# Kernel tuning notes

Measured on AMD Instinct MI355X. Metric: run time of the kernel, lower is better.

## Reference

```python
import jax, jax.numpy as jnp
import numpy as np

OUT, GROUPS, GRID = 4096, 1, 8   # 2^bits = 8 -> 3-bit codes
IN = 4096
B, S = 4, 2048

def setup_inputs() -> dict:
    key = jax.random.key(0)
    k1, k2, k3 = jax.random.split(key, 3)
    x = jax.random.normal(k1, (B, S, IN), dtype=jnp.float32)
    quant_grid = jax.random.normal(k2, (OUT, GROUPS, GRID), dtype=jnp.float32) * 0.02
    weight_codes = jax.random.randint(k3, (OUT, GROUPS, IN // GROUPS), 0, GRID, dtype=jnp.int32)
    return {"x": x, "quant_grid": quant_grid, "weight_codes": weight_codes}

def reference(x, quant_grid, weight_codes):
    # Dequantize: per-(row, group) codebook lookup -> full weight [OUT, IN]
    W = jnp.take_along_axis(quant_grid, weight_codes, axis=-1)  # [OUT, GROUPS, IN//GROUPS]
    W = W.reshape(W.shape[0], -1)                               # [OUT, IN]
    # y = X @ W.T
    return jnp.einsum('bsi,oi->bso', x, W)
```

## Files before the change

kernel.cpp:

```cpp
#include <hip/hip_runtime.h>


#define M_DIM 8192
#define N_DIM 4096
#define K_DIM 4096
#define BK 64
#define NKT (K_DIM / BK)

typedef __attribute__((ext_vector_type(4))) int int32x4;

#define AS1 __attribute__((address_space(1)))
#define AS3 __attribute__((address_space(3)))

__device__ __forceinline__ void gl_lds16(const void* g, void* l) {
    __builtin_amdgcn_global_load_lds((const AS1 void*)g, (AS3 void*)l, 16, 0, 0);
}

__global__ __launch_bounds__(256) void quant_x(const float* __restrict__ X,
                                               char* __restrict__ XQ,
                                               float* __restrict__ SX) {
    const int row = blockIdx.x;
    const int t = threadIdx.x;
    const float4* xp = (const float4*)(X + (size_t)row * K_DIM);
    float4 v[4];
    float mx = 0.0f;
#pragma unroll
    for (int i = 0; i < 4; ++i) {
        v[i] = xp[t * 4 + i];
        mx = fmaxf(mx, fmaxf(fmaxf(fabsf(v[i].x), fabsf(v[i].y)),
                             fmaxf(fabsf(v[i].z), fabsf(v[i].w))));
    }
#pragma unroll
    for (int off = 1; off < 64; off <<= 1)
        mx = fmaxf(mx, __shfl_xor(mx, off));
    __shared__ float wmx[4];
    if ((t & 63) == 0) wmx[t >> 6] = mx;
    __syncthreads();
    mx = fmaxf(fmaxf(wmx[0], wmx[1]), fmaxf(wmx[2], wmx[3]));
    const float inv = 127.0f / mx;
    int4 o4;
    int* po = (int*)&o4;
#pragma unroll
    for (int i = 0; i < 4; ++i) {
        int q0 = (int)rintf(v[i].x * inv);
        int q1 = (int)rintf(v[i].y * inv);
        int q2 = (int)rintf(v[i].z * inv);
        int q3 = (int)rintf(v[i].w * inv);
        po[i] = (q0 & 255) | ((q1 & 255) << 8) | ((q2 & 255) << 16) | ((q3 & 255) << 24);
    }
    const int mpanel = row >> 6, mf = (row >> 4) & 3, fr = row & 15;
    const int kp = t >> 2, kg = t & 3;
    ((int4*)XQ)[(size_t)mpanel * 16384 + kp * 256 + mf * 64 + kg * 16 + fr] = o4;
    if (t == 0) SX[row] = mx * (1.0f / 127.0f);
}

__global__ __launch_bounds__(256) void quant_w(const int* __restrict__ CD,
                                               const float* __restrict__ G,
                                               char* __restrict__ WQ,
                                               float* __restrict__ SW) {
    const int o = blockIdx.x;
    __shared__ int gq[8];
    if (threadIdx.x == 0) {
        float g[8], mx = 0.0f;
#pragma unroll
        for (int j = 0; j < 8; ++j) { g[j] = G[o * 8 + j]; mx = fmaxf(mx, fabsf(g[j])); }
        mx = fmaxf(mx, 1e-20f);
        const float inv = 127.0f / mx;
        SW[o] = mx * (1.0f / 127.0f);
#pragma unroll
        for (int j = 0; j < 8; ++j) gq[j] = ((int)rintf(g[j] * inv)) & 255;
    }
    __syncthreads();
    const int4* cp = (const int4*)(CD + (size_t)o * K_DIM);
    int* wp = (int*)(WQ + (size_t)o * K_DIM);
#pragma unroll
    for (int r = 0; r < 4; ++r) {
        int idx = r * 256 + threadIdx.x;
        int4 c = cp[idx];
        wp[idx] = gq[c.x] | (gq[c.y] << 8) | (gq[c.z] << 16) | (gq[c.w] << 24);
    }
}

__global__ __launch_bounds__(512, 4) void gemm8(const char* __restrict__ A,
                                                const char* __restrict__ B,
                                                const float* __restrict__ SX,
                                                const float* __restrict__ SW,
                                                float* __restrict__ C) {
    __shared__ char Bs[2][256 * 64];

    const int tid = threadIdx.x;
    const int lane = tid & 63;
    const int wid = tid >> 6;
    const int wm = wid >> 2;
    const int wn = wid & 3;

    int wg = blockIdx.x;
    wg = (wg & 7) * (gridDim.x >> 3) + (wg >> 3);
    const int ntn = N_DIM / 256;
    const int bm = (wg / ntn) * 128;
    const int bn = (wg % ntn) * 256;

    const int fr = lane & 15;
    const int g = lane >> 4;
    const int offk = fr * 64 + ((g ^ ((fr >> 1) & 3)) << 4);
    const int bwoff = wn * 4096;

    const char* Apan = A + (size_t)((bm >> 6) + wm) * 262144 + lane * 16;

    const int row0 = tid >> 2;
    const int sl = (((tid & 3) ^ ((row0 >> 1) & 3)) << 4);
    const char* gB0 = B + (size_t)(bn + row0) * K_DIM + sl;
    const char* gB1 = B + (size_t)(bn + 128 + row0) * K_DIM + sl;

#define KCL(KT) (((KT) < NKT) ? (KT) : 0)

#define STGB(BUF, KT) do {                                                         \
        const int kb_ = KCL(KT) * BK;                                              \
        gl_lds16(gB0 + kb_, &Bs[BUF][0] + wid * 1024);                             \
        gl_lds16(gB1 + kb_, &Bs[BUF][8192] + wid * 1024);                          \
    } while (0)

#define LDA(KT) do {                                                               \
        const char* ap_ = Apan + (size_t)KCL(KT) * 4096;                           \
        fa[0] = *(const int32x4*)(ap_);                                            \
        fa[1] = *(const int32x4*)(ap_ + 1024);                                     \
        fa[2] = *(const int32x4*)(ap_ + 2048);                                     \
        fa[3] = *(const int32x4*)(ap_ + 3072);                                     \
    } while (0)

#define RD_B(BUF)                                                                  \
    _Pragma("unroll") for (int n = 0; n < 4; ++n)                                  \
        fb[n] = *(const int32x4*)&Bs[BUF][bwoff + n * 1024 + offk];

#define MF_ALL                                                                     \
    _Pragma("unroll") for (int m = 0; m < 4; ++m)                                  \
    _Pragma("unroll") for (int n = 0; n < 4; ++n)                                  \
        acc[m][n] = __builtin_amdgcn_mfma_i32_16x16x64_i8(fa[m], fb[n], acc[m][n], 0, 0, 0);

#define BODY(CUR, KT) do {                                                         \
        RD_B(CUR)                                                                  \
        __builtin_amdgcn_s_setprio(1);                                             \
        MF_ALL                                                                     \
        __builtin_amdgcn_s_setprio(0);                                             \
        __builtin_amdgcn_sched_barrier(0);                                         \
        LDA((KT) + 1);                                                             \
        asm volatile("s_waitcnt vmcnt(4)" ::: "memory");                           \
        __builtin_amdgcn_s_barrier();                                              \
        STGB(CUR, (KT) + 2);                                                       \
    } while (0)

    int32x4 acc[4][4] = {};
    int32x4 fa[4];
    int32x4 fb[4];

    STGB(0, 0);
    STGB(1, 1);
    LDA(0);
    asm volatile("s_waitcnt vmcnt(4)" ::: "memory");
    __builtin_amdgcn_s_barrier();

    for (int j = 0; j < NKT / 2; ++j) {
        BODY(0, 2 * j);
        BODY(1, 2 * j + 1);
    }
    asm volatile("s_waitcnt vmcnt(0)" ::: "memory");

    const int crow0 = bm + wm * 64 + (g << 2);
    const int ccol0 = bn + wn * 64 + fr;
    float swc[4];
#pragma unroll
    for (int ni = 0; ni < 4; ++ni) swc[ni] = SW[ccol0 + ni * 16];
#pragma unroll
    for (int mi = 0; mi < 4; ++mi)
#pragma unroll
        for (int r = 0; r < 4; ++r) {
            const float sxr = SX[crow0 + mi * 16 + r];
#pragma unroll
            for (int ni = 0; ni < 4; ++ni)
                C[(size_t)(crow0 + mi * 16 + r) * N_DIM + ccol0 + ni * 16] =
                    (float)acc[mi][ni][r] * sxr * swc[ni];
        }
}

__global__ __launch_bounds__(256) void fb_gemm(const float* __restrict__ X,
                                               const float* __restrict__ G,
                                               const int* __restrict__ CD,
                                               float* __restrict__ Y) {
    __shared__ float xs[16][64];
    __shared__ float ws[16][64];
    const int bm = blockIdx.y << 6, bn = blockIdx.x << 6;
    const int tid = threadIdx.x;
    const int tn = tid & 15, tm = tid >> 4;
    float acc[4][4] = {};
    for (int k0 = 0; k0 < K_DIM; k0 += 16) {
#pragma unroll
        for (int r = 0; r < 4; ++r) {
            int e = r * 256 + tid;
            int mm = e >> 4, kk = e & 15;
            xs[kk][mm] = X[(size_t)(bm + mm) * K_DIM + k0 + kk];
            int code = CD[(size_t)(bn + mm) * K_DIM + k0 + kk];
            ws[kk][mm] = G[(bn + mm) * 8 + code];
        }
        __syncthreads();
#pragma unroll
        for (int kk = 0; kk < 16; ++kk)
#pragma unroll
            for (int i = 0; i < 4; ++i)
#pragma unroll
                for (int j = 0; j < 4; ++j)
                    acc[i][j] += xs[kk][tm * 4 + i] * ws[kk][tn * 4 + j];
        __syncthreads();
    }
#pragma unroll
    for (int i = 0; i < 4; ++i)
#pragma unroll
        for (int j = 0; j < 4; ++j)
            Y[(size_t)(bm + tm * 4 + i) * N_DIM + bn + tn * 4 + j] = acc[i][j];
}

extern "C" void kernel_launch(void* const* d_in, const int* in_sizes, int n_in,
                              void* d_out, int out_size, void* d_ws, size_t ws_size,
                              hipStream_t stream) {
    const float* x = (const float*)d_in[0];
    const float* qg = (const float*)d_in[1];
    const int* wc = (const int*)d_in[2];
    float* y = (float*)d_out;

    const size_t sx_off = 0;
    const size_t sw_off = (size_t)M_DIM * 4;
    const size_t xq_off = (size_t)(M_DIM + N_DIM) * 4;
    const size_t wq_off = xq_off + (size_t)M_DIM * K_DIM;
    const size_t need = wq_off + (size_t)N_DIM * K_DIM;

    if (ws_size >= need) {
        float* sx = (float*)((char*)d_ws + sx_off);
        float* sw = (float*)((char*)d_ws + sw_off);
        char* xq = (char*)d_ws + xq_off;
        char* wq = (char*)d_ws + wq_off;
        hipLaunchKernelGGL(quant_x, dim3(M_DIM), dim3(256), 0, stream, x, xq, sx);
        hipLaunchKernelGGL(quant_w, dim3(N_DIM), dim3(256), 0, stream, wc, qg, wq, sw);
        const int nwg = (M_DIM / 128) * (N_DIM / 256);
        hipLaunchKernelGGL(gemm8, dim3(nwg), dim3(512), 0, stream,
                           xq, wq, sx, sw, y);
    } else {
        hipLaunchKernelGGL(fb_gemm, dim3(N_DIM / 64, M_DIM / 64), dim3(256), 0, stream,
                           x, qg, wc, y);
    }
}
```

Before: 221.2 us.

## Stage A through LDS with 256x256 tiles and triple-buffered pipeline

```diff
diff --git a/kernel.cpp b/kernel.cpp
--- a/kernel.cpp
+++ b/kernel.cpp
@@ -48,9 +48,7 @@
         int q3 = (int)rintf(v[i].w * inv);
         po[i] = (q0 & 255) | ((q1 & 255) << 8) | ((q2 & 255) << 16) | ((q3 & 255) << 24);
     }
-    const int mpanel = row >> 6, mf = (row >> 4) & 3, fr = row & 15;
-    const int kp = t >> 2, kg = t & 3;
-    ((int4*)XQ)[(size_t)mpanel * 16384 + kp * 256 + mf * 64 + kg * 16 + fr] = o4;
+    ((int4*)(XQ + (size_t)row * K_DIM))[t] = o4;
     if (t == 0) SX[row] = mx * (1.0f / 127.0f);
 }
 
@@ -81,12 +79,14 @@
     }
 }
 
-__global__ __launch_bounds__(512, 4) void gemm8(const char* __restrict__ A,
+__global__ __launch_bounds__(512, 2) void gemm3(const char* __restrict__ A,
                                                 const char* __restrict__ B,
                                                 const float* __restrict__ SX,
                                                 const float* __restrict__ SW,
                                                 float* __restrict__ C) {
-    __shared__ char Bs[2][256 * 64];
+    __shared__ char As[3][256 * 64];
+    __shared__ char Bs[3][256 * 64];
+    __shared__ char Scr[16384];
 
     const int tid = threadIdx.x;
     const int lane = tid & 63;
@@ -97,81 +97,69 @@
     int wg = blockIdx.x;
     wg = (wg & 7) * (gridDim.x >> 3) + (wg >> 3);
     const int ntn = N_DIM / 256;
-    const int bm = (wg / ntn) * 128;
+    const int bm = (wg / ntn) * 256;
     const int bn = (wg % ntn) * 256;
 
     const int fr = lane & 15;
     const int g = lane >> 4;
     const int offk = fr * 64 + ((g ^ ((fr >> 1) & 3)) << 4);
-    const int bwoff = wn * 4096;
-
-    const char* Apan = A + (size_t)((bm >> 6) + wm) * 262144 + lane * 16;
 
     const int row0 = tid >> 2;
     const int sl = (((tid & 3) ^ ((row0 >> 1) & 3)) << 4);
+    const char* gA0 = A + (size_t)(bm + row0) * K_DIM + sl;
+    const char* gA1 = A + (size_t)(bm + 128 + row0) * K_DIM + sl;
     const char* gB0 = B + (size_t)(bn + row0) * K_DIM + sl;
     const char* gB1 = B + (size_t)(bn + 128 + row0) * K_DIM + sl;
 
-#define KCL(KT) (((KT) < NKT) ? (KT) : 0)
-
-#define STGB(BUF, KT) do {                                                         \
-        const int kb_ = KCL(KT) * BK;                                              \
-        gl_lds16(gB0 + kb_, &Bs[BUF][0] + wid * 1024);                             \
-        gl_lds16(gB1 + kb_, &Bs[BUF][8192] + wid * 1024);                          \
+#define STG_TO(DA, DB, KT) do {                                                    \
+        const int kb_ = (KT) * BK;                                                 \
+        gl_lds16(gA0 + kb_, (DA) + wid * 1024);                                    \
+        gl_lds16(gA1 + kb_, (DA) + 8192 + wid * 1024);                             \
+        gl_lds16(gB0 + kb_, (DB) + wid * 1024);                                    \
+        gl_lds16(gB1 + kb_, (DB) + 8192 + wid * 1024);                             \
     } while (0)
 
-#define LDA(KT) do {                                                               \
-        const char* ap_ = Apan + (size_t)KCL(KT) * 4096;                           \
-        fa[0] = *(const int32x4*)(ap_);                                            \
-        fa[1] = *(const int32x4*)(ap_ + 1024);                                     \
-        fa[2] = *(const int32x4*)(ap_ + 2048);                                     \
-        fa[3] = *(const int32x4*)(ap_ + 3072);                                     \
-    } while (0)
-
-#define RD_B(BUF)                                                                  \
-    _Pragma("unroll") for (int n = 0; n < 4; ++n)                                  \
-        fb[n] = *(const int32x4*)&Bs[BUF][bwoff + n * 1024 + offk];
-
-#define MF_ALL                                                                     \
-    _Pragma("unroll") for (int m = 0; m < 4; ++m)                                  \
-    _Pragma("unroll") for (int n = 0; n < 4; ++n)                                  \
-        acc[m][n] = __builtin_amdgcn_mfma_i32_16x16x64_i8(fa[m], fb[n], acc[m][n], 0, 0, 0);
-
-#define BODY(CUR, KT) do {                                                         \
-        RD_B(CUR)                                                                  \
-        __builtin_amdgcn_s_setprio(1);                                             \
-        MF_ALL                                                                     \
-        __builtin_amdgcn_s_setprio(0);                                             \
-        __builtin_amdgcn_sched_barrier(0);                                         \
-        LDA((KT) + 1);                                                             \
-        asm volatile("s_waitcnt vmcnt(4)" ::: "memory");                           \
-        __builtin_amdgcn_s_barrier();                                              \
-        STGB(CUR, (KT) + 2);                                                       \
-    } while (0)
-
-    int32x4 acc[4][4] = {};
-    int32x4 fa[4];
+    int32x4 acc[8][4] = {};
+    int32x4 fa[8];
     int32x4 fb[4];
 
-    STGB(0, 0);
-    STGB(1, 1);
-    LDA(0);
+    STG_TO(&As[0][0], &Bs[0][0], 0);
+    STG_TO(&As[1][0], &Bs[1][0], 1);
     asm volatile("s_waitcnt vmcnt(4)" ::: "memory");
     __builtin_amdgcn_s_barrier();
 
-    for (int j = 0; j < NKT / 2; ++j) {
-        BODY(0, 2 * j);
-        BODY(1, 2 * j + 1);
+    for (int t = 0; t < NKT; ++t) {
+        const int cur = t % 3;
+        {
+            const int s = t + 2;
+            char* da = (s < NKT) ? &As[s % 3][0] : &Scr[0];
+            char* db = (s < NKT) ? &Bs[s % 3][0] : &Scr[0];
+            STG_TO(da, db, (s < NKT) ? s : 0);
+        }
+#pragma unroll
+        for (int m = 0; m < 8; ++m)
+            fa[m] = *(const int32x4*)&As[cur][wm * 8192 + m * 1024 + offk];
+#pragma unroll
+        for (int n = 0; n < 4; ++n)
+            fb[n] = *(const int32x4*)&Bs[cur][wn * 4096 + n * 1024 + offk];
+#pragma unroll
+        for (int m = 0; m < 8; ++m)
+#pragma unroll
+            for (int n = 0; n < 4; ++n)
+                acc[m][n] = __builtin_amdgcn_mfma_i32_16x16x64_i8(
+                    fa[m], fb[n], acc[m][n], 0, 0, 0);
+        asm volatile("s_waitcnt vmcnt(4)" ::: "memory");
+        __builtin_amdgcn_s_barrier();
     }
     asm volatile("s_waitcnt vmcnt(0)" ::: "memory");
 
-    const int crow0 = bm + wm * 64 + (g << 2);
+    const int crow0 = bm + wm * 128 + (g << 2);
     const int ccol0 = bn + wn * 64 + fr;
     float swc[4];
 #pragma unroll
     for (int ni = 0; ni < 4; ++ni) swc[ni] = SW[ccol0 + ni * 16];
 #pragma unroll
-    for (int mi = 0; mi < 4; ++mi)
+    for (int mi = 0; mi < 8; ++mi)
 #pragma unroll
         for (int r = 0; r < 4; ++r) {
             const float sxr = SX[crow0 + mi * 16 + r];
@@ -239,8 +227,8 @@
         char* wq = (char*)d_ws + wq_off;
         hipLaunchKernelGGL(quant_x, dim3(M_DIM), dim3(256), 0, stream, x, xq, sx);
         hipLaunchKernelGGL(quant_w, dim3(N_DIM), dim3(256), 0, stream, wc, qg, wq, sw);
-        const int nwg = (M_DIM / 128) * (N_DIM / 256);
-        hipLaunchKernelGGL(gemm8, dim3(nwg), dim3(512), 0, stream,
+        const int nwg = (M_DIM / 256) * (N_DIM / 256);
+        hipLaunchKernelGGL(gemm3, dim3(nwg), dim3(512), 0, stream,
                            xq, wq, sx, sw, y);
     } else {
         hipLaunchKernelGGL(fb_gemm, dim3(N_DIM / 64, M_DIM / 64), dim3(256), 0, stream,
```

Result: faster. 210.7 us (-4.7%).

## Stage both GEMM operands through LDS with triple buffering and 256x128 tiles

Applied to the files above, without the earlier changes.

```diff
diff --git a/kernel.cpp b/kernel.cpp
--- a/kernel.cpp
+++ b/kernel.cpp
@@ -48,9 +48,7 @@
         int q3 = (int)rintf(v[i].w * inv);
         po[i] = (q0 & 255) | ((q1 & 255) << 8) | ((q2 & 255) << 16) | ((q3 & 255) << 24);
     }
-    const int mpanel = row >> 6, mf = (row >> 4) & 3, fr = row & 15;
-    const int kp = t >> 2, kg = t & 3;
-    ((int4*)XQ)[(size_t)mpanel * 16384 + kp * 256 + mf * 64 + kg * 16 + fr] = o4;
+    ((int4*)(XQ + (size_t)row * K_DIM))[t] = o4;
     if (t == 0) SX[row] = mx * (1.0f / 127.0f);
 }
 
@@ -81,97 +79,102 @@
     }
 }
 
-__global__ __launch_bounds__(512, 4) void gemm8(const char* __restrict__ A,
+__global__ __launch_bounds__(256, 2) void gemm3(const char* __restrict__ A,
                                                 const char* __restrict__ B,
                                                 const float* __restrict__ SX,
                                                 const float* __restrict__ SW,
                                                 float* __restrict__ C) {
-    __shared__ char Bs[2][256 * 64];
+    __shared__ char As[3][256 * 64];
+    __shared__ char Bs[3][128 * 64];
 
     const int tid = threadIdx.x;
     const int lane = tid & 63;
     const int wid = tid >> 6;
-    const int wm = wid >> 2;
-    const int wn = wid & 3;
+    const int wm = wid >> 1;
+    const int wn = wid & 1;
 
     int wg = blockIdx.x;
     wg = (wg & 7) * (gridDim.x >> 3) + (wg >> 3);
-    const int ntn = N_DIM / 256;
-    const int bm = (wg / ntn) * 128;
-    const int bn = (wg % ntn) * 256;
+    const int ntn = N_DIM / 128;
+    const int bm = (wg / ntn) * 256;
+    const int bn = (wg % ntn) * 128;
 
     const int fr = lane & 15;
     const int g = lane >> 4;
     const int offk = fr * 64 + ((g ^ ((fr >> 1) & 3)) << 4);
+    const int awoff = wm * 8192;
     const int bwoff = wn * 4096;
-
-    const char* Apan = A + (size_t)((bm >> 6) + wm) * 262144 + lane * 16;
 
     const int row0 = tid >> 2;
     const int sl = (((tid & 3) ^ ((row0 >> 1) & 3)) << 4);
+    const char* gA0 = A + (size_t)(bm + row0) * K_DIM + sl;
+    const char* gA1 = A + (size_t)(bm + 64 + row0) * K_DIM + sl;
+    const char* gA2 = A + (size_t)(bm + 128 + row0) * K_DIM + sl;
+    const char* gA3 = A + (size_t)(bm + 192 + row0) * K_DIM + sl;
     const char* gB0 = B + (size_t)(bn + row0) * K_DIM + sl;
-    const char* gB1 = B + (size_t)(bn + 128 + row0) * K_DIM + sl;
+    const char* gB1 = B + (size_t)(bn + 64 + row0) * K_DIM + sl;
 
 #define KCL(KT) (((KT) < NKT) ? (KT) : 0)
 
-#define STGB(BUF, KT) do {                                                         \
+#define STG(BUF, KT) do {                                                          \
         const int kb_ = KCL(KT) * BK;                                              \
-        gl_lds16(gB0 + kb_, &Bs[BUF][0] + wid * 1024);                             \
-        gl_lds16(gB1 + kb_, &Bs[BUF][8192] + wid * 1024);                          \
+        gl_lds16(gA0 + kb_, &As[BUF][0] + tid * 16);                               \
+        gl_lds16(gA1 + kb_, &As[BUF][4096] + tid * 16);                            \
+        gl_lds16(gA2 + kb_, &As[BUF][8192] + tid * 16);                            \
+        gl_lds16(gA3 + kb_, &As[BUF][12288] + tid * 16);                           \
+        gl_lds16(gB0 + kb_, &Bs[BUF][0] + tid * 16);                               \
+        gl_lds16(gB1 + kb_, &Bs[BUF][4096] + tid * 16);                            \
     } while (0)
 
-#define LDA(KT) do {                                                               \
-        const char* ap_ = Apan + (size_t)KCL(KT) * 4096;                           \
-        fa[0] = *(const int32x4*)(ap_);                                            \
-        fa[1] = *(const int32x4*)(ap_ + 1024);                                     \
-        fa[2] = *(const int32x4*)(ap_ + 2048);                                     \
-        fa[3] = *(const int32x4*)(ap_ + 3072);                                     \
-    } while (0)
-
-#define RD_B(BUF)                                                                  \
+#define RD_B(CUR)                                                                  \
     _Pragma("unroll") for (int n = 0; n < 4; ++n)                                  \
-        fb[n] = *(const int32x4*)&Bs[BUF][bwoff + n * 1024 + offk];
+        fb[n] = *(const int32x4*)&Bs[CUR][bwoff + n * 1024 + offk];
+
+#define RD_A(CUR)                                                                  \
+    _Pragma("unroll") for (int m = 0; m < 8; ++m)                                  \
+        fa[m] = *(const int32x4*)&As[CUR][awoff + m * 1024 + offk];
 
 #define MF_ALL                                                                     \
-    _Pragma("unroll") for (int m = 0; m < 4; ++m)                                  \
+    _Pragma("unroll") for (int m = 0; m < 8; ++m)                                  \
     _Pragma("unroll") for (int n = 0; n < 4; ++n)                                  \
         acc[m][n] = __builtin_amdgcn_mfma_i32_16x16x64_i8(fa[m], fb[n], acc[m][n], 0, 0, 0);
 
-#define BODY(CUR, KT) do {                                                         \
-        RD_B(CUR)                                                                  \
+#define BODY(CUR, NXT2, T) do {                                                    \
+        STG(NXT2, (T) + 2);                                                        \
+        RD_B(CUR) RD_A(CUR)                                                        \
         __builtin_amdgcn_s_setprio(1);                                             \
         MF_ALL                                                                     \
         __builtin_amdgcn_s_setprio(0);                                             \
         __builtin_amdgcn_sched_barrier(0);                                         \
-        LDA((KT) + 1);                                                             \
-        asm volatile("s_waitcnt vmcnt(4)" ::: "memory");                           \
+        asm volatile("s_waitcnt vmcnt(6)" ::: "memory");                           \
         __builtin_amdgcn_s_barrier();                                              \
-        STGB(CUR, (KT) + 2);                                                       \
     } while (0)
 
-    int32x4 acc[4][4] = {};
-    int32x4 fa[4];
+    int32x4 acc[8][4] = {};
+    int32x4 fa[8];
     int32x4 fb[4];
 
-    STGB(0, 0);
-    STGB(1, 1);
-    LDA(0);
-    asm volatile("s_waitcnt vmcnt(4)" ::: "memory");
+    STG(0, 0);
+    STG(1, 1);
+    asm volatile("s_waitcnt vmcnt(6)" ::: "memory");
     __builtin_amdgcn_s_barrier();
 
-    for (int j = 0; j < NKT / 2; ++j) {
-        BODY(0, 2 * j);
-        BODY(1, 2 * j + 1);
-    }
+    for (int j = 0; j < 21; ++j) {
+        const int t = 3 * j;
+        BODY(0, 2, t);
+        BODY(1, 0, t + 1);
+        BODY(2, 1, t + 2);
+    }
+    BODY(0, 2, 63);
     asm volatile("s_waitcnt vmcnt(0)" ::: "memory");
 
-    const int crow0 = bm + wm * 64 + (g << 2);
+    const int crow0 = bm + wm * 128 + (g << 2);
     const int ccol0 = bn + wn * 64 + fr;
     float swc[4];
 #pragma unroll
     for (int ni = 0; ni < 4; ++ni) swc[ni] = SW[ccol0 + ni * 16];
 #pragma unroll
-    for (int mi = 0; mi < 4; ++mi)
+    for (int mi = 0; mi < 8; ++mi)
 #pragma unroll
         for (int r = 0; r < 4; ++r) {
             const float sxr = SX[crow0 + mi * 16 + r];
@@ -239,8 +242,8 @@
         char* wq = (char*)d_ws + wq_off;
         hipLaunchKernelGGL(quant_x, dim3(M_DIM), dim3(256), 0, stream, x, xq, sx);
         hipLaunchKernelGGL(quant_w, dim3(N_DIM), dim3(256), 0, stream, wc, qg, wq, sw);
-        const int nwg = (M_DIM / 128) * (N_DIM / 256);
-        hipLaunchKernelGGL(gemm8, dim3(nwg), dim3(512), 0, stream,
+        const int nwg = (M_DIM / 256) * (N_DIM / 128);
+        hipLaunchKernelGGL(gemm3, dim3(nwg), dim3(256), 0, stream,
                            xq, wq, sx, sw, y);
     } else {
         hipLaunchKernelGGL(fb_gemm, dim3(N_DIM / 64, M_DIM / 64), dim3(256), 0, stream,
```

After: 205.2 us. 7.2% less time.
